# Performance work log

Hardware: AMD Instinct MI355X
Metric: run time of the kernel (lower is better)

Reference implementation:

```python
import jax, jax.numpy as jnp
import numpy as np

B, N, D_IN, D_OUT = 4, 2048, 1024, 1024


def setup_inputs() -> dict:
    key = jax.random.key(0)
    kx, kq, kk, kv = jax.random.split(key, 4)
    x = jax.random.normal(kx, (B, N, D_IN), dtype=jnp.float32)
    # torch Linear(d_in, d_out, bias=False): y = x @ W.T, W ~ U(-1/sqrt(d_in), 1/sqrt(d_in)).
    # Store as [d_in, d_out] so y = x @ W.
    bound = 1.0 / np.sqrt(D_IN)
    Wq = jax.random.uniform(kq, (D_IN, D_OUT), jnp.float32, -bound, bound)
    Wk = jax.random.uniform(kk, (D_IN, D_OUT), jnp.float32, -bound, bound)
    Wv = jax.random.uniform(kv, (D_IN, D_OUT), jnp.float32, -bound, bound)
    return {"x": x, "Wq": Wq, "Wk": Wk, "Wv": Wv}


def reference(x, Wq, Wk, Wv):
    # x: [B, N, d_in]
    q = jnp.einsum("bnd,de->bne", x, Wq)  # [B, N, d_out]
    k = jnp.einsum("bnd,de->bne", x, Wk)
    v = jnp.einsum("bnd,de->bne", x, Wv)
    n = x.shape[1]
    scores = jnp.einsum("bqe,bke->bqk", q, k)  # [B, N, N]
    causal = jnp.triu(jnp.ones((n, n), dtype=bool), k=1)  # True above diagonal -> masked
    scores = jnp.where(causal, -jnp.inf, scores)
    scale = 1.0 / jnp.sqrt(jnp.asarray(k.shape[-1], dtype=scores.dtype))
    weights = jax.nn.softmax(scores * scale, axis=-1)
    # dropout with drop_rate=0.0 is identity
    return jnp.einsum("bqk,bke->bqe", weights, v)  # [B, N, d_out]
```

## Files before the change

kernel.cpp:

```cpp
#include <hip/hip_runtime.h>

typedef float  f4v  __attribute__((ext_vector_type(4)));
typedef short  s8v  __attribute__((ext_vector_type(8)));

__device__ __forceinline__ ushort f2b(float f) {
    union { float f; unsigned int u; } v; v.f = f;
    unsigned int u = v.u;
    u += 0x7fffu + ((u >> 16) & 1u);
    return (ushort)(u >> 16);
}
__device__ __forceinline__ float b2f(ushort u) {
    union { unsigned int u; float f; } v; v.u = ((unsigned int)u) << 16;
    return v.f;
}

__device__ __forceinline__ void async16(const ushort* g, ushort* ldsp) {
    __builtin_amdgcn_global_load_lds(
        (const __attribute__((address_space(1))) unsigned int*)g,
        (__attribute__((address_space(3))) unsigned int*)ldsp, 16, 0, 0);
}

__global__ __launch_bounds__(256) void prep(const float* __restrict__ in,
                                            ushort* __restrict__ out,
                                            float* __restrict__ l,
                                            const float* __restrict__ w0,
                                            const float* __restrict__ w1,
                                            const float* __restrict__ w2,
                                            ushort* __restrict__ wt) {
    const int L = blockIdx.x, tid = threadIdx.x;
    if (L < 8192) {
        int i = L * 256 + tid;
        if (i < 8192) l[i] = 0.f;
        float4 f = ((const float4*)in)[i];
        ushort4 o;
        o.x = f2b(f.x); o.y = f2b(f.y); o.z = f2b(f.z); o.w = f2b(f.w);
        ((ushort4*)out)[i] = o;
        return;
    }
    __shared__ float tile[32][33];
    const int T = L - 8192;
    const int z = T >> 10, rem = T & 1023;
    const int bx = rem & 31, by = rem >> 5;
    const float* W = (z == 0) ? w0 : (z == 1 ? w1 : w2);
    ushort* O = wt + (size_t)z * (1024u * 1024u);
    int x0 = bx * 32, y0 = by * 32;
    int tx = tid & 31, ty = tid >> 5;
    for (int i = 0; i < 4; i++)
        tile[ty + i * 8][tx] = W[(size_t)(y0 + ty + i * 8) * 1024 + x0 + tx];
    __syncthreads();
    for (int i = 0; i < 4; i++)
        O[(size_t)(x0 + ty + i * 8) * 1024 + y0 + tx] = f2b(tile[tx][ty + i * 8]);
}


#define RD_A4(buf_)                                                                   \
    _Pragma("unroll") for (int mi = 0; mi < 4; mi++)                                  \
    _Pragma("unroll") for (int s = 0; s < 2; s++)                                     \
        af[mi][s] = *(const s8v*)&(buf_)[(wm + mi * 16 + l16) * 64 +                  \
                                         (((s * 4 + quad) ^ (l16 & 7)) * 8)];

#define RD_B2(buf_, NI0_)                                                             \
    _Pragma("unroll") for (int j = 0; j < 2; j++)                                     \
    _Pragma("unroll") for (int s = 0; s < 2; s++)                                     \
        bf[j][s] = *(const s8v*)&(buf_)[(wn + ((NI0_) + j) * 16 + l16) * 64 +         \
                                        (((s * 4 + quad) ^ (l16 & 7)) * 8)];

#define MFMA16(NI0_)                                                                  \
    _Pragma("unroll") for (int mi = 0; mi < 4; mi++)                                  \
    _Pragma("unroll") for (int j = 0; j < 2; j++)                                     \
    _Pragma("unroll") for (int s = 0; s < 2; s++)                                     \
        acc[mi][(NI0_) + j] = __builtin_amdgcn_mfma_f32_16x16x32_bf16(                \
            af[mi][s], bf[j][s], acc[mi][(NI0_) + j], 0, 0, 0);

__global__ __launch_bounds__(512, 2) void gemm_qkv(const ushort* __restrict__ A,
                                                   const ushort* __restrict__ Wt,
                                                   ushort* __restrict__ q,
                                                   ushort* __restrict__ k,
                                                   ushort* __restrict__ vt) {
    constexpr int K = 1024;
    extern __shared__ ushort lds[];

    const int L = blockIdx.x;
    const int xcd = L & 7, idx = L >> 3;
    const int ci = xcd >> 1, cj = xcd & 1;
    const int mo = idx >> 3, no = idx & 7;
    const int m0 = (ci * 8 + mo) * 256;
    const int n0 = (cj * 8 + no) * 192;

    const int tid = threadIdx.x;
    const int w = tid >> 6, lane = tid & 63, quad = lane >> 4, l16 = lane & 15;
    const int wm = (w >> 1) * 64, wn = (w & 1) * 96;

    ushort* a0 = lds;
    ushort* a1 = lds + 16384;
    ushort* a2 = lds + 32768;
    ushort* b0 = lds + 49152;
    ushort* b1 = lds + 61440;

    const int lr = lane >> 3;
    const int lc8 = (lane & 7) ^ lr;
    const ushort* Ab = A  + (size_t)(m0 + w * 8 + lr) * K + lc8 * 8;
    const ushort* Bb = Wt + (size_t)(n0 + w * 8 + lr) * K + lc8 * 8;
    const int dW = w * 512;

#define ISSUE_A(buf_, kk_, a_) async16(Ab + (size_t)(a_) * 64 * K + (kk_), (buf_) + (a_) * 4096 + dW)
#define ISSUE_B(buf_, kk_, c_) async16(Bb + (size_t)(c_) * 64 * K + (kk_), (buf_) + (c_) * 4096 + dW)

    f4v acc[4][6];
    #pragma unroll
    for (int mi = 0; mi < 4; mi++)
        #pragma unroll
        for (int ni = 0; ni < 6; ni++) acc[mi][ni] = 0;

    #pragma unroll
    for (int a = 0; a < 4; a++) ISSUE_A(a0, 0, a);
    #pragma unroll
    for (int c = 0; c < 3; c++) ISSUE_B(b0, 0, c);
    #pragma unroll
    for (int a = 0; a < 4; a++) ISSUE_A(a1, 64, a);
    asm volatile("s_waitcnt vmcnt(4)" ::: "memory");
    asm volatile("s_barrier" ::: "memory");

    for (int t = 0; t < 16; ++t) {
        const int kB = (t + 1) * 64;
        const int kA = (t + 2) * 64;
        s8v af[4][2], bf[2][2];

        RD_A4(a0)
        RD_B2(b0, 0)
        if (t < 15) {
            ISSUE_B(b1, kB, 0);
            ISSUE_B(b1, kB, 1);
            ISSUE_B(b1, kB, 2);
        }
        asm volatile("s_barrier" ::: "memory");
        __builtin_amdgcn_s_setprio(1);
        MFMA16(0)
        __builtin_amdgcn_s_setprio(0);
        asm volatile("s_barrier" ::: "memory");

        RD_B2(b0, 2)
        if (t < 14) {
            ISSUE_A(a2, kA, 0);
            ISSUE_A(a2, kA, 1);
        }
        asm volatile("s_barrier" ::: "memory");
        __builtin_amdgcn_s_setprio(1);
        MFMA16(2)
        __builtin_amdgcn_s_setprio(0);
        asm volatile("s_barrier" ::: "memory");

        RD_B2(b0, 4)
        if (t < 14) {
            ISSUE_A(a2, kA, 2);
            ISSUE_A(a2, kA, 3);
        }
        asm volatile("s_barrier" ::: "memory");
        __builtin_amdgcn_s_setprio(1);
        MFMA16(4)
        __builtin_amdgcn_s_setprio(0);

        if (t < 14)       asm volatile("s_waitcnt vmcnt(4)" ::: "memory");
        else if (t == 14) asm volatile("s_waitcnt vmcnt(0)" ::: "memory");
        asm volatile("s_barrier" ::: "memory");

        ushort* ta = a0; a0 = a1; a1 = a2; a2 = ta;
        ushort* tb = b0; b0 = b1; b1 = tb;
    }

    #pragma unroll
    for (int mi = 0; mi < 4; mi++)
        #pragma unroll
        for (int ni = 0; ni < 6; ni++) {
            int row = m0 + wm + mi * 16 + quad * 4;
            int col = n0 + wn + ni * 16 + l16;
            int z = col >> 10, cz = col & 1023;
            f4v v = acc[mi][ni];
            if (z < 2) {
                ushort* C = (z == 0) ? q : k;
                #pragma unroll
                for (int rr = 0; rr < 4; rr++)
                    C[(size_t)(row + rr) * 1024 + cz] = f2b(v[rr]);
            } else {
                int b = row >> 11, tok = row & 2047;
                ushort4 pk;
                pk.x = f2b(v[0]); pk.y = f2b(v[1]); pk.z = f2b(v[2]); pk.w = f2b(v[3]);
                *(ushort4*)&vt[(size_t)b * (1024u * 2048u) + (size_t)cz * 2048 + tok] = pk;
            }
        }
#undef ISSUE_A
#undef ISSUE_B
}

__global__ __launch_bounds__(512, 2) void sgemm_qk(const ushort* __restrict__ Q,
                                                   const ushort* __restrict__ Km,
                                                   ushort* __restrict__ E,
                                                   float* __restrict__ l) {
    constexpr int K = 1024;
    extern __shared__ ushort lds[];

    const int L = blockIdx.x;
    const int xcd = L & 7, i = L >> 3;
    const int t = (xcd < 4) ? (xcd * 26 + i) : (104 + (xcd - 4) * 25 + i);
    const int b = t / 51;
    int tt = t - b * 51;
    int mt = 0;
    for (;; mt++) {
        int c = (4 * (mt + 1) + 2) / 3;
        if (tt < c) break;
        tt -= c;
    }
    const int nt = tt;
    const int m0 = mt * 256, n0 = nt * 192;
    const ushort* A  = Q  + (size_t)b * 2048 * 1024;
    const ushort* Bt = Km + (size_t)b * 2048 * 1024;
    ushort* Cb = E + (size_t)b * 2048 * 2048;
    float* lb = l + (size_t)b * 2048;

    const int tid = threadIdx.x;
    const int w = tid >> 6, lane = tid & 63, quad = lane >> 4, l16 = lane & 15;
    const int wm = (w >> 1) * 64, wn = (w & 1) * 96;

    ushort* a0 = lds;
    ushort* a1 = lds + 16384;
    ushort* a2 = lds + 32768;
    ushort* b0 = lds + 49152;
    ushort* b1 = lds + 61440;

    const int lr = lane >> 3;
    const int lc8 = (lane & 7) ^ lr;
    const ushort* Ab = A  + (size_t)(m0 + w * 8 + lr) * K + lc8 * 8;
    const ushort* Bb = Bt + (size_t)(n0 + w * 8 + lr) * K + lc8 * 8;
    const int dW = w * 512;

#define ISSUE_A(buf_, kk_, a_) async16(Ab + (size_t)(a_) * 64 * K + (kk_), (buf_) + (a_) * 4096 + dW)
#define ISSUE_B(buf_, kk_, c_) async16(Bb + (size_t)(c_) * 64 * K + (kk_), (buf_) + (c_) * 4096 + dW)

    f4v acc[4][6];
    #pragma unroll
    for (int mi = 0; mi < 4; mi++)
        #pragma unroll
        for (int ni = 0; ni < 6; ni++) acc[mi][ni] = 0;

    #pragma unroll
    for (int a = 0; a < 4; a++) ISSUE_A(a0, 0, a);
    #pragma unroll
    for (int c = 0; c < 3; c++) ISSUE_B(b0, 0, c);
    #pragma unroll
    for (int a = 0; a < 4; a++) ISSUE_A(a1, 64, a);
    asm volatile("s_waitcnt vmcnt(4)" ::: "memory");
    asm volatile("s_barrier" ::: "memory");

    for (int tk = 0; tk < 16; ++tk) {
        const int kB = (tk + 1) * 64;
        const int kA = (tk + 2) * 64;
        s8v af[4][2], bf[2][2];

        RD_A4(a0)
        RD_B2(b0, 0)
        if (tk < 15) {
            ISSUE_B(b1, kB, 0);
            ISSUE_B(b1, kB, 1);
            ISSUE_B(b1, kB, 2);
        }
        asm volatile("s_barrier" ::: "memory");
        __builtin_amdgcn_s_setprio(1);
        MFMA16(0)
        __builtin_amdgcn_s_setprio(0);
        asm volatile("s_barrier" ::: "memory");

        RD_B2(b0, 2)
        if (tk < 14) {
            ISSUE_A(a2, kA, 0);
            ISSUE_A(a2, kA, 1);
        }
        asm volatile("s_barrier" ::: "memory");
        __builtin_amdgcn_s_setprio(1);
        MFMA16(2)
        __builtin_amdgcn_s_setprio(0);
        asm volatile("s_barrier" ::: "memory");

        RD_B2(b0, 4)
        if (tk < 14) {
            ISSUE_A(a2, kA, 2);
            ISSUE_A(a2, kA, 3);
        }
        asm volatile("s_barrier" ::: "memory");
        __builtin_amdgcn_s_setprio(1);
        MFMA16(4)
        __builtin_amdgcn_s_setprio(0);

        if (tk < 14)       asm volatile("s_waitcnt vmcnt(4)" ::: "memory");
        else if (tk == 14) asm volatile("s_waitcnt vmcnt(0)" ::: "memory");
        asm volatile("s_barrier" ::: "memory");

        ushort* ta = a0; a0 = a1; a1 = a2; a2 = ta;
        ushort* tb = b0; b0 = b1; b1 = tb;
    }

    #pragma unroll
    for (int mi = 0; mi < 4; mi++) {
        float rs[4] = {0.f, 0.f, 0.f, 0.f};
        #pragma unroll
        for (int ni = 0; ni < 6; ni++) {
            const int colbase = n0 + wn + ni * 16;
            if (colbase >= 2048) continue;
            const int col = colbase + l16;
            f4v v = acc[mi][ni];
            #pragma unroll
            for (int rr = 0; rr < 4; rr++) {
                const int row = m0 + wm + mi * 16 + quad * 4 + rr;
                float e = (col <= row) ? __expf(v[rr] * 0.03125f) : 0.f;
                ushort eb = f2b(e);
                Cb[(size_t)row * 2048 + col] = eb;
                rs[rr] += b2f(eb);
            }
        }
        #pragma unroll
        for (int rr = 0; rr < 4; rr++) {
            float s = rs[rr];
            s += __shfl_xor(s, 1);
            s += __shfl_xor(s, 2);
            s += __shfl_xor(s, 4);
            s += __shfl_xor(s, 8);
            if (l16 == 0)
                atomicAdd(&lb[m0 + wm + mi * 16 + quad * 4 + rr], s);
        }
    }
#undef ISSUE_A
#undef ISSUE_B
}

__global__ __launch_bounds__(512, 2) void gemm_pv(const ushort* __restrict__ Em,
                                                  const ushort* __restrict__ Vt,
                                                  const float* __restrict__ l,
                                                  float* __restrict__ Out) {
    extern __shared__ ushort lds[];
    const int L = blockIdx.x;
    const int p = (L & 7) * 32 + (L >> 3);
    const int pair = p >> 5;
    const int inner = p & 31;
    const int b = inner >> 3;
    const int nt = inner & 7;
    const int n0 = nt * 128;
    const ushort* A  = Em + (size_t)b * 2048 * 2048;
    const ushort* Bt = Vt + (size_t)b * 1024 * 2048;
    const float* lb = l + (size_t)b * 2048;
    float* C = Out + (size_t)b * 2048 * 1024;

    const int tid = threadIdx.x;
    const int w = tid >> 6, lane = tid & 63, quad = lane >> 4, l16 = lane & 15;
    const int wm = (w >> 2) * 64, wn = (w & 3) * 32;

    const int lr = lane >> 3;
    const int lc8 = (lane & 7) ^ lr;
    const int dW = w * 512;

#define ISSUE_A(buf_, kk_, a_) async16(Ab + (size_t)(a_) * 64 * 2048 + (kk_), (buf_) + (a_) * 4096 + dW)
#define ISSUE_B(buf_, kk_, c_) async16(Bb + (size_t)(c_) * 64 * 2048 + (kk_), (buf_) + (c_) * 4096 + dW)

    #pragma unroll
    for (int half = 0; half < 2; ++half) {
        const int mt = half ? (15 - pair) : pair;
        const int m0 = mt * 128;
        const int NT = 2 * (mt + 1);

        ushort* a0 = lds;
        ushort* a1 = lds + 8192;
        ushort* a2 = lds + 16384;
        ushort* b0 = lds + 24576;
        ushort* b1 = lds + 32768;

        const ushort* Ab = A  + (size_t)(m0 + w * 8 + lr) * 2048 + lc8 * 8;
        const ushort* Bb = Bt + (size_t)(n0 + w * 8 + lr) * 2048 + lc8 * 8;

        f4v acc[4][2];
        #pragma unroll
        for (int mi = 0; mi < 4; mi++)
            #pragma unroll
            for (int ni = 0; ni < 2; ni++) acc[mi][ni] = 0;

        #pragma unroll
        for (int a = 0; a < 2; a++) ISSUE_A(a0, 0, a);
        #pragma unroll
        for (int c = 0; c < 2; c++) ISSUE_B(b0, 0, c);
        #pragma unroll
        for (int a = 0; a < 2; a++) ISSUE_A(a1, 64, a);
        asm volatile("s_waitcnt vmcnt(2)" ::: "memory");
        asm volatile("s_barrier" ::: "memory");

        for (int tk = 0; tk < NT; ++tk) {
            const int kB = (tk + 1) * 64;
            const int kA = (tk + 2) * 64;
            s8v af[4][2], bf[2][2];

            RD_A4(a0)
            RD_B2(b0, 0)
            if (tk < NT - 1) {
                ISSUE_B(b1, kB, 0);
                ISSUE_B(b1, kB, 1);
            }
            if (tk < NT - 2) {
                ISSUE_A(a2, kA, 0);
                ISSUE_A(a2, kA, 1);
            }
            asm volatile("s_barrier" ::: "memory");
            __builtin_amdgcn_s_setprio(1);
            MFMA16(0)
            __builtin_amdgcn_s_setprio(0);

            if (tk < NT - 2)       asm volatile("s_waitcnt vmcnt(2)" ::: "memory");
            else if (tk == NT - 2) asm volatile("s_waitcnt vmcnt(0)" ::: "memory");
            asm volatile("s_barrier" ::: "memory");

            ushort* ta = a0; a0 = a1; a1 = a2; a2 = ta;
            ushort* tb = b0; b0 = b1; b1 = tb;
        }

        #pragma unroll
        for (int mi = 0; mi < 4; mi++) {
            const int row = m0 + wm + mi * 16 + quad * 4;
            float inv[4];
            #pragma unroll
            for (int rr = 0; rr < 4; rr++) inv[rr] = 1.f / lb[row + rr];
            #pragma unroll
            for (int ni = 0; ni < 2; ni++) {
                const int col = n0 + wn + ni * 16 + l16;
                f4v v = acc[mi][ni];
                #pragma unroll
                for (int rr = 0; rr < 4; rr++)
                    C[(size_t)(row + rr) * 1024 + col] = v[rr] * inv[rr];
            }
        }
    }
#undef ISSUE_A
#undef ISSUE_B
}

extern "C" void kernel_launch(void* const* d_in, const int* in_sizes, int n_in,
                              void* d_out, int out_size, void* d_ws, size_t ws_size,
                              hipStream_t stream) {
    const float* x  = (const float*)d_in[0];
    const float* Wq = (const float*)d_in[1];
    const float* Wk = (const float*)d_in[2];
    const float* Wv = (const float*)d_in[3];
    float* out = (float*)d_out;

    static bool init = false;
    if (!init) {
        hipFuncSetAttribute(reinterpret_cast<const void*>(gemm_qkv),
                            hipFuncAttributeMaxDynamicSharedMemorySize, 147456);
        hipFuncSetAttribute(reinterpret_cast<const void*>(sgemm_qk),
                            hipFuncAttributeMaxDynamicSharedMemorySize, 147456);
        hipFuncSetAttribute(reinterpret_cast<const void*>(gemm_pv),
                            hipFuncAttributeMaxDynamicSharedMemorySize, 81920);
        init = true;
    }

    char* ws = (char*)d_ws;
    const size_t MiB = 1u << 20;
    ushort* xb = (ushort*)(ws);
    ushort* wt = (ushort*)(ws + 16 * MiB);
    ushort* q  = (ushort*)(ws + 22 * MiB);
    ushort* k  = (ushort*)(ws + 38 * MiB);
    ushort* vt = (ushort*)(ws + 54 * MiB);
    ushort* E  = (ushort*)(ws + 70 * MiB);
    float*  l  = (float*)(ws + 102 * MiB);

    prep<<<8192 + 3072, 256, 0, stream>>>(x, xb, l, Wq, Wk, Wv, wt);

    gemm_qkv<<<512, 512, 147456, stream>>>(xb, wt, q, k, vt);
    sgemm_qk<<<204, 512, 147456, stream>>>(q, k, E, l);
    gemm_pv<<<256, 512, 81920, stream>>>(E, vt, l, out);
}
```

Before: 214.6 us.

## Double-buffer register fragments to prefetch next LDS tile during MFMAs

The three GEMM main loops are restructured so that the A (and in gemm_pv the B) fragments for the next k-tile are read from LDS into a second register set while the current tile's MFMAs run, using ping-pong register arrays and a loop unrolled by two. gemm_pv also gains a third B LDS buffer so both A and B are triple-buffered, which raises its dynamic LDS size and changes its waitcnt and barrier schedule. The aim is to hide LDS read latency behind matrix-core work and to cut barriers. In exchange, register pressure rises, which could cause spills at the given launch bounds, and the hand-tuned vmcnt values must exactly match the new issue order.

```diff
diff --git a/kernel.cpp b/kernel.cpp
--- a/kernel.cpp
+++ b/kernel.cpp
@@ -53,24 +53,70 @@
 }
 
 
-#define RD_A4(buf_)                                                                   \
+#define RD_A4_TO(dst_, buf_)                                                          \
     _Pragma("unroll") for (int mi = 0; mi < 4; mi++)                                  \
     _Pragma("unroll") for (int s = 0; s < 2; s++)                                     \
-        af[mi][s] = *(const s8v*)&(buf_)[(wm + mi * 16 + l16) * 64 +                  \
-                                         (((s * 4 + quad) ^ (l16 & 7)) * 8)];
-
-#define RD_B2(buf_, NI0_)                                                             \
+        dst_[mi][s] = *(const s8v*)&(buf_)[(wm + mi * 16 + l16) * 64 +                \
+                                           (((s * 4 + quad) ^ (l16 & 7)) * 8)];
+
+#define RD_B2_TO(dst_, buf_, NI0_)                                                    \
     _Pragma("unroll") for (int j = 0; j < 2; j++)                                     \
     _Pragma("unroll") for (int s = 0; s < 2; s++)                                     \
-        bf[j][s] = *(const s8v*)&(buf_)[(wn + ((NI0_) + j) * 16 + l16) * 64 +         \
-                                        (((s * 4 + quad) ^ (l16 & 7)) * 8)];
-
-#define MFMA16(NI0_)                                                                  \
+        dst_[j][s] = *(const s8v*)&(buf_)[(wn + ((NI0_) + j) * 16 + l16) * 64 +       \
+                                          (((s * 4 + quad) ^ (l16 & 7)) * 8)];
+
+#define MFMA16F(af_, bf_, NI0_)                                                       \
     _Pragma("unroll") for (int mi = 0; mi < 4; mi++)                                  \
     _Pragma("unroll") for (int j = 0; j < 2; j++)                                     \
     _Pragma("unroll") for (int s = 0; s < 2; s++)                                     \
         acc[mi][(NI0_) + j] = __builtin_amdgcn_mfma_f32_16x16x32_bf16(                \
-            af[mi][s], bf[j][s], acc[mi][(NI0_) + j], 0, 0, 0);
+            af_[mi][s], bf_[j][s], acc[mi][(NI0_) + j], 0, 0, 0);
+
+#define TILE3(t_, AFC_, AFN_)                                                         \
+  {                                                                                   \
+    const int kB = ((t_) + 1) * 64;                                                   \
+    const int kA = ((t_) + 2) * 64;                                                   \
+    s8v bf0[2][2], bf1[2][2], bf2[2][2];                                              \
+    RD_B2_TO(bf0, b0, 0)                                                              \
+    if ((t_) < 15) {                                                                  \
+        ISSUE_B(b1, kB, 0);                                                           \
+        ISSUE_B(b1, kB, 1);                                                           \
+        ISSUE_B(b1, kB, 2);                                                           \
+    }                                                                                 \
+    RD_B2_TO(bf1, b0, 2)                                                              \
+    asm volatile("s_barrier" ::: "memory");                                           \
+    __builtin_amdgcn_s_setprio(1);                                                    \
+    MFMA16F(AFC_, bf0, 0)                                                             \
+    __builtin_amdgcn_s_setprio(0);                                                    \
+    asm volatile("s_barrier" ::: "memory");                                           \
+    if ((t_) < 14) {                                                                  \
+        ISSUE_A(a2, kA, 0);                                                           \
+        ISSUE_A(a2, kA, 1);                                                           \
+        asm volatile("s_waitcnt vmcnt(5)" ::: "memory");                              \
+    } else {                                                                          \
+        asm volatile("s_waitcnt vmcnt(3)" ::: "memory");                              \
+    }                                                                                 \
+    RD_B2_TO(bf2, b0, 4)                                                              \
+    asm volatile("s_barrier" ::: "memory");                                           \
+    __builtin_amdgcn_s_setprio(1);                                                    \
+    MFMA16F(AFC_, bf1, 2)                                                             \
+    __builtin_amdgcn_s_setprio(0);                                                    \
+    asm volatile("s_barrier" ::: "memory");                                           \
+    if ((t_) < 14) {                                                                  \
+        ISSUE_A(a2, kA, 2);                                                           \
+        ISSUE_A(a2, kA, 3);                                                           \
+    }                                                                                 \
+    RD_A4_TO(AFN_, a1)                                                                \
+    asm volatile("s_barrier" ::: "memory");                                           \
+    __builtin_amdgcn_s_setprio(1);                                                    \
+    MFMA16F(AFC_, bf2, 4)                                                             \
+    __builtin_amdgcn_s_setprio(0);                                                    \
+    if ((t_) < 14)       asm volatile("s_waitcnt vmcnt(4)" ::: "memory");             \
+    else if ((t_) == 14) asm volatile("s_waitcnt vmcnt(0)" ::: "memory");             \
+    asm volatile("s_barrier" ::: "memory");                                           \
+    ushort* ta = a0; a0 = a1; a1 = a2; a2 = ta;                                       \
+    ushort* tb = b0; b0 = b1; b1 = tb;                                                \
+  }
 
 __global__ __launch_bounds__(512, 2) void gemm_qkv(const ushort* __restrict__ A,
                                                    const ushort* __restrict__ Wt,
@@ -121,51 +167,11 @@
     asm volatile("s_waitcnt vmcnt(4)" ::: "memory");
     asm volatile("s_barrier" ::: "memory");
 
-    for (int t = 0; t < 16; ++t) {
-        const int kB = (t + 1) * 64;
-        const int kA = (t + 2) * 64;
-        s8v af[4][2], bf[2][2];
-
-        RD_A4(a0)
-        RD_B2(b0, 0)
-        if (t < 15) {
-            ISSUE_B(b1, kB, 0);
-            ISSUE_B(b1, kB, 1);
-            ISSUE_B(b1, kB, 2);
-        }
-        asm volatile("s_barrier" ::: "memory");
-        __builtin_amdgcn_s_setprio(1);
-        MFMA16(0)
-        __builtin_amdgcn_s_setprio(0);
-        asm volatile("s_barrier" ::: "memory");
-
-        RD_B2(b0, 2)
-        if (t < 14) {
-            ISSUE_A(a2, kA, 0);
-            ISSUE_A(a2, kA, 1);
-        }
-        asm volatile("s_barrier" ::: "memory");
-        __builtin_amdgcn_s_setprio(1);
-        MFMA16(2)
-        __builtin_amdgcn_s_setprio(0);
-        asm volatile("s_barrier" ::: "memory");
-
-        RD_B2(b0, 4)
-        if (t < 14) {
-            ISSUE_A(a2, kA, 2);
-            ISSUE_A(a2, kA, 3);
-        }
-        asm volatile("s_barrier" ::: "memory");
-        __builtin_amdgcn_s_setprio(1);
-        MFMA16(4)
-        __builtin_amdgcn_s_setprio(0);
-
-        if (t < 14)       asm volatile("s_waitcnt vmcnt(4)" ::: "memory");
-        else if (t == 14) asm volatile("s_waitcnt vmcnt(0)" ::: "memory");
-        asm volatile("s_barrier" ::: "memory");
-
-        ushort* ta = a0; a0 = a1; a1 = a2; a2 = ta;
-        ushort* tb = b0; b0 = b1; b1 = tb;
+    s8v afX[4][2], afY[4][2];
+    RD_A4_TO(afX, a0)
+    for (int tp = 0; tp < 8; ++tp) {
+        TILE3(2 * tp,     afX, afY)
+        TILE3(2 * tp + 1, afY, afX)
     }
 
     #pragma unroll
@@ -251,51 +257,11 @@
     asm volatile("s_waitcnt vmcnt(4)" ::: "memory");
     asm volatile("s_barrier" ::: "memory");
 
-    for (int tk = 0; tk < 16; ++tk) {
-        const int kB = (tk + 1) * 64;
-        const int kA = (tk + 2) * 64;
-        s8v af[4][2], bf[2][2];
-
-        RD_A4(a0)
-        RD_B2(b0, 0)
-        if (tk < 15) {
-            ISSUE_B(b1, kB, 0);
-            ISSUE_B(b1, kB, 1);
-            ISSUE_B(b1, kB, 2);
-        }
-        asm volatile("s_barrier" ::: "memory");
-        __builtin_amdgcn_s_setprio(1);
-        MFMA16(0)
-        __builtin_amdgcn_s_setprio(0);
-        asm volatile("s_barrier" ::: "memory");
-
-        RD_B2(b0, 2)
-        if (tk < 14) {
-            ISSUE_A(a2, kA, 0);
-            ISSUE_A(a2, kA, 1);
-        }
-        asm volatile("s_barrier" ::: "memory");
-        __builtin_amdgcn_s_setprio(1);
-        MFMA16(2)
-        __builtin_amdgcn_s_setprio(0);
-        asm volatile("s_barrier" ::: "memory");
-
-        RD_B2(b0, 4)
-        if (tk < 14) {
-            ISSUE_A(a2, kA, 2);
-            ISSUE_A(a2, kA, 3);
-        }
-        asm volatile("s_barrier" ::: "memory");
-        __builtin_amdgcn_s_setprio(1);
-        MFMA16(4)
-        __builtin_amdgcn_s_setprio(0);
-
-        if (tk < 14)       asm volatile("s_waitcnt vmcnt(4)" ::: "memory");
-        else if (tk == 14) asm volatile("s_waitcnt vmcnt(0)" ::: "memory");
-        asm volatile("s_barrier" ::: "memory");
-
-        ushort* ta = a0; a0 = a1; a1 = a2; a2 = ta;
-        ushort* tb = b0; b0 = b1; b1 = tb;
+    s8v afX[4][2], afY[4][2];
+    RD_A4_TO(afX, a0)
+    for (int tp = 0; tp < 8; ++tp) {
+        TILE3(2 * tp,     afX, afY)
+        TILE3(2 * tp + 1, afY, afX)
     }
 
     #pragma unroll
@@ -359,6 +325,26 @@
 #define ISSUE_A(buf_, kk_, a_) async16(Ab + (size_t)(a_) * 64 * 2048 + (kk_), (buf_) + (a_) * 4096 + dW)
 #define ISSUE_B(buf_, kk_, c_) async16(Bb + (size_t)(c_) * 64 * 2048 + (kk_), (buf_) + (c_) * 4096 + dW)
 
+#define TILE1(t_, FCA_, FCB_, FNA_, FNB_)                                             \
+  {                                                                                   \
+    const int kk = ((t_) + 2) * 64;                                                   \
+    if ((t_) < NT - 2) {                                                              \
+        ISSUE_A(a2, kk, 0); ISSUE_A(a2, kk, 1);                                       \
+        ISSUE_B(b2, kk, 0); ISSUE_B(b2, kk, 1);                                       \
+        asm volatile("s_waitcnt vmcnt(4)" ::: "memory");                              \
+    } else if ((t_) == NT - 2) {                                                      \
+        asm volatile("s_waitcnt vmcnt(0)" ::: "memory");                              \
+    }                                                                                 \
+    asm volatile("s_barrier" ::: "memory");                                           \
+    RD_A4_TO(FNA_, a1)                                                                \
+    RD_B2_TO(FNB_, b1, 0)                                                             \
+    __builtin_amdgcn_s_setprio(1);                                                    \
+    MFMA16F(FCA_, FCB_, 0)                                                            \
+    __builtin_amdgcn_s_setprio(0);                                                    \
+    ushort* ta = a0; a0 = a1; a1 = a2; a2 = ta;                                       \
+    ushort* tb = b0; b0 = b1; b1 = b2; b2 = tb;                                       \
+  }
+
     #pragma unroll
     for (int half = 0; half < 2; ++half) {
         const int mt = half ? (15 - pair) : pair;
@@ -370,6 +356,7 @@
         ushort* a2 = lds + 16384;
         ushort* b0 = lds + 24576;
         ushort* b1 = lds + 32768;
+        ushort* b2 = lds + 40960;
 
         const ushort* Ab = A  + (size_t)(m0 + w * 8 + lr) * 2048 + lc8 * 8;
         const ushort* Bb = Bt + (size_t)(n0 + w * 8 + lr) * 2048 + lc8 * 8;
@@ -380,41 +367,21 @@
             #pragma unroll
             for (int ni = 0; ni < 2; ni++) acc[mi][ni] = 0;
 
-        #pragma unroll
-        for (int a = 0; a < 2; a++) ISSUE_A(a0, 0, a);
-        #pragma unroll
-        for (int c = 0; c < 2; c++) ISSUE_B(b0, 0, c);
-        #pragma unroll
-        for (int a = 0; a < 2; a++) ISSUE_A(a1, 64, a);
-        asm volatile("s_waitcnt vmcnt(2)" ::: "memory");
         asm volatile("s_barrier" ::: "memory");
 
-        for (int tk = 0; tk < NT; ++tk) {
-            const int kB = (tk + 1) * 64;
-            const int kA = (tk + 2) * 64;
-            s8v af[4][2], bf[2][2];
-
-            RD_A4(a0)
-            RD_B2(b0, 0)
-            if (tk < NT - 1) {
-                ISSUE_B(b1, kB, 0);
-                ISSUE_B(b1, kB, 1);
-            }
-            if (tk < NT - 2) {
-                ISSUE_A(a2, kA, 0);
-                ISSUE_A(a2, kA, 1);
-            }
-            asm volatile("s_barrier" ::: "memory");
-            __builtin_amdgcn_s_setprio(1);
-            MFMA16(0)
-            __builtin_amdgcn_s_setprio(0);
-
-            if (tk < NT - 2)       asm volatile("s_waitcnt vmcnt(2)" ::: "memory");
-            else if (tk == NT - 2) asm volatile("s_waitcnt vmcnt(0)" ::: "memory");
-            asm volatile("s_barrier" ::: "memory");
-
-            ushort* ta = a0; a0 = a1; a1 = a2; a2 = ta;
-            ushort* tb = b0; b0 = b1; b1 = tb;
+        ISSUE_A(a0, 0, 0); ISSUE_A(a0, 0, 1);
+        ISSUE_B(b0, 0, 0); ISSUE_B(b0, 0, 1);
+        ISSUE_A(a1, 64, 0); ISSUE_A(a1, 64, 1);
+        ISSUE_B(b1, 64, 0); ISSUE_B(b1, 64, 1);
+        asm volatile("s_waitcnt vmcnt(4)" ::: "memory");
+        asm volatile("s_barrier" ::: "memory");
+
+        s8v afX[4][2], bfX[2][2], afY[4][2], bfY[2][2];
+        RD_A4_TO(afX, a0)
+        RD_B2_TO(bfX, b0, 0)
+        for (int tk = 0; tk < NT; tk += 2) {
+            TILE1(tk,     afX, bfX, afY, bfY)
+            TILE1(tk + 1, afY, bfY, afX, bfX)
         }
 
         #pragma unroll
@@ -433,6 +400,7 @@
             }
         }
     }
+#undef TILE1
 #undef ISSUE_A
 #undef ISSUE_B
 }
@@ -453,7 +421,7 @@
         hipFuncSetAttribute(reinterpret_cast<const void*>(sgemm_qk),
                             hipFuncAttributeMaxDynamicSharedMemorySize, 147456);
         hipFuncSetAttribute(reinterpret_cast<const void*>(gemm_pv),
-                            hipFuncAttributeMaxDynamicSharedMemorySize, 81920);
+                            hipFuncAttributeMaxDynamicSharedMemorySize, 98304);
         init = true;
     }
 
@@ -471,5 +439,5 @@
 
     gemm_qkv<<<512, 512, 147456, stream>>>(xb, wt, q, k, vt);
     sgemm_qk<<<204, 512, 147456, stream>>>(q, k, E, l);
-    gemm_pv<<<256, 512, 81920, stream>>>(E, vt, l, out);
-}
+    gemm_pv<<<256, 512, 98304, stream>>>(E, vt, l, out);
+}
```

Result: faster. 209.3 us (-2.5%).

## Triple-buffer B and double-buffer register fragments in gemm_pv main loop

Applied to the files above, without the earlier changes.

The PV GEMM main loop is rewritten so both A and B tiles use three LDS buffers, with a single barrier per k-step instead of two. Register fragments are ping-ponged, so the next tile's LDS reads run while the current tile's MFMAs execute. The aim is to cut barrier stalls and hide LDS read latency behind matrix math. In exchange, dynamic LDS grows to 96 KiB and register pressure rises. The loop is unrolled by two, which assumes NT is even; NT = 2*(mt+1) satisfies this.

```diff
diff --git a/kernel.cpp b/kernel.cpp
--- a/kernel.cpp
+++ b/kernel.cpp
@@ -72,6 +72,25 @@
         acc[mi][(NI0_) + j] = __builtin_amdgcn_mfma_f32_16x16x32_bf16(                \
             af[mi][s], bf[j][s], acc[mi][(NI0_) + j], 0, 0, 0);
 
+#define RD_A4_TO(dst_, buf_)                                                          \
+    _Pragma("unroll") for (int mi = 0; mi < 4; mi++)                                  \
+    _Pragma("unroll") for (int s = 0; s < 2; s++)                                     \
+        dst_[mi][s] = *(const s8v*)&(buf_)[(wm + mi * 16 + l16) * 64 +                \
+                                           (((s * 4 + quad) ^ (l16 & 7)) * 8)];
+
+#define RD_B2_TO(dst_, buf_, NI0_)                                                    \
+    _Pragma("unroll") for (int j = 0; j < 2; j++)                                     \
+    _Pragma("unroll") for (int s = 0; s < 2; s++)                                     \
+        dst_[j][s] = *(const s8v*)&(buf_)[(wn + ((NI0_) + j) * 16 + l16) * 64 +       \
+                                          (((s * 4 + quad) ^ (l16 & 7)) * 8)];
+
+#define MFMA16F(af_, bf_, NI0_)                                                       \
+    _Pragma("unroll") for (int mi = 0; mi < 4; mi++)                                  \
+    _Pragma("unroll") for (int j = 0; j < 2; j++)                                     \
+    _Pragma("unroll") for (int s = 0; s < 2; s++)                                     \
+        acc[mi][(NI0_) + j] = __builtin_amdgcn_mfma_f32_16x16x32_bf16(                \
+            af_[mi][s], bf_[j][s], acc[mi][(NI0_) + j], 0, 0, 0);
+
 __global__ __launch_bounds__(512, 2) void gemm_qkv(const ushort* __restrict__ A,
                                                    const ushort* __restrict__ Wt,
                                                    ushort* __restrict__ q,
@@ -359,6 +378,26 @@
 #define ISSUE_A(buf_, kk_, a_) async16(Ab + (size_t)(a_) * 64 * 2048 + (kk_), (buf_) + (a_) * 4096 + dW)
 #define ISSUE_B(buf_, kk_, c_) async16(Bb + (size_t)(c_) * 64 * 2048 + (kk_), (buf_) + (c_) * 4096 + dW)
 
+#define TILE1(t_, FCA_, FCB_, FNA_, FNB_)                                             \
+  {                                                                                   \
+    const int kk = ((t_) + 2) * 64;                                                   \
+    if ((t_) < NT - 2) {                                                              \
+        ISSUE_A(a2, kk, 0); ISSUE_A(a2, kk, 1);                                       \
+        ISSUE_B(b2, kk, 0); ISSUE_B(b2, kk, 1);                                       \
+        asm volatile("s_waitcnt vmcnt(4)" ::: "memory");                              \
+    } else if ((t_) == NT - 2) {                                                      \
+        asm volatile("s_waitcnt vmcnt(0)" ::: "memory");                              \
+    }                                                                                 \
+    asm volatile("s_barrier" ::: "memory");                                           \
+    RD_A4_TO(FNA_, a1)                                                                \
+    RD_B2_TO(FNB_, b1, 0)                                                             \
+    __builtin_amdgcn_s_setprio(1);                                                    \
+    MFMA16F(FCA_, FCB_, 0)                                                            \
+    __builtin_amdgcn_s_setprio(0);                                                    \
+    ushort* ta = a0; a0 = a1; a1 = a2; a2 = ta;                                       \
+    ushort* tb = b0; b0 = b1; b1 = b2; b2 = tb;                                       \
+  }
+
     #pragma unroll
     for (int half = 0; half < 2; ++half) {
         const int mt = half ? (15 - pair) : pair;
@@ -370,6 +409,7 @@
         ushort* a2 = lds + 16384;
         ushort* b0 = lds + 24576;
         ushort* b1 = lds + 32768;
+        ushort* b2 = lds + 40960;
 
         const ushort* Ab = A  + (size_t)(m0 + w * 8 + lr) * 2048 + lc8 * 8;
         const ushort* Bb = Bt + (size_t)(n0 + w * 8 + lr) * 2048 + lc8 * 8;
@@ -380,41 +420,21 @@
             #pragma unroll
             for (int ni = 0; ni < 2; ni++) acc[mi][ni] = 0;
 
-        #pragma unroll
-        for (int a = 0; a < 2; a++) ISSUE_A(a0, 0, a);
-        #pragma unroll
-        for (int c = 0; c < 2; c++) ISSUE_B(b0, 0, c);
-        #pragma unroll
-        for (int a = 0; a < 2; a++) ISSUE_A(a1, 64, a);
-        asm volatile("s_waitcnt vmcnt(2)" ::: "memory");
-        asm volatile("s_barrier" ::: "memory");
-
-        for (int tk = 0; tk < NT; ++tk) {
-            const int kB = (tk + 1) * 64;
-            const int kA = (tk + 2) * 64;
-            s8v af[4][2], bf[2][2];
-
-            RD_A4(a0)
-            RD_B2(b0, 0)
-            if (tk < NT - 1) {
-                ISSUE_B(b1, kB, 0);
-                ISSUE_B(b1, kB, 1);
-            }
-            if (tk < NT - 2) {
-                ISSUE_A(a2, kA, 0);
-                ISSUE_A(a2, kA, 1);
-            }
-            asm volatile("s_barrier" ::: "memory");
-            __builtin_amdgcn_s_setprio(1);
-            MFMA16(0)
-            __builtin_amdgcn_s_setprio(0);
-
-            if (tk < NT - 2)       asm volatile("s_waitcnt vmcnt(2)" ::: "memory");
-            else if (tk == NT - 2) asm volatile("s_waitcnt vmcnt(0)" ::: "memory");
-            asm volatile("s_barrier" ::: "memory");
-
-            ushort* ta = a0; a0 = a1; a1 = a2; a2 = ta;
-            ushort* tb = b0; b0 = b1; b1 = tb;
+        asm volatile("s_barrier" ::: "memory");
+
+        ISSUE_A(a0, 0, 0); ISSUE_A(a0, 0, 1);
+        ISSUE_B(b0, 0, 0); ISSUE_B(b0, 0, 1);
+        ISSUE_A(a1, 64, 0); ISSUE_A(a1, 64, 1);
+        ISSUE_B(b1, 64, 0); ISSUE_B(b1, 64, 1);
+        asm volatile("s_waitcnt vmcnt(4)" ::: "memory");
+        asm volatile("s_barrier" ::: "memory");
+
+        s8v afX[4][2], bfX[2][2], afY[4][2], bfY[2][2];
+        RD_A4_TO(afX, a0)
+        RD_B2_TO(bfX, b0, 0)
+        for (int tk = 0; tk < NT; tk += 2) {
+            TILE1(tk,     afX, bfX, afY, bfY)
+            TILE1(tk + 1, afY, bfY, afX, bfX)
         }
 
         #pragma unroll
@@ -433,6 +453,7 @@
             }
         }
     }
+#undef TILE1
 #undef ISSUE_A
 #undef ISSUE_B
 }
@@ -453,7 +474,7 @@
         hipFuncSetAttribute(reinterpret_cast<const void*>(sgemm_qk),
                             hipFuncAttributeMaxDynamicSharedMemorySize, 147456);
         hipFuncSetAttribute(reinterpret_cast<const void*>(gemm_pv),
-                            hipFuncAttributeMaxDynamicSharedMemorySize, 81920);
+                            hipFuncAttributeMaxDynamicSharedMemorySize, 98304);
         init = true;
     }
 
@@ -471,5 +492,5 @@
 
     gemm_qkv<<<512, 512, 147456, stream>>>(xb, wt, q, k, vt);
     sgemm_qk<<<204, 512, 147456, stream>>>(q, k, E, l);
-    gemm_pv<<<256, 512, 81920, stream>>>(E, vt, l, out);
-}
+    gemm_pv<<<256, 512, 98304, stream>>>(E, vt, l, out);
+}
```

New measurement: 207.6 us. -3.2%, faster.
